# Kernel optimization log

Measured on AMD Instinct MI355X. Metric: run time of the kernel, lower is better.

## Reference

```python
import jax, jax.numpy as jnp
import numpy as np

HEAD_N = 16
EMBED_D = 1024
MASK_FILL = 1e-09  # source uses masked_fill(mask==0, 1e-09), NOT -inf


def setup_inputs() -> dict:
    key = jax.random.key(0)
    ks = jax.random.split(key, 8)
    B, S, D = 4, 4096, EMBED_D
    L = S // HEAD_N
    q = jax.random.normal(ks[0], (B, S, D), dtype=jnp.float32)
    k = jax.random.normal(ks[1], (B, S, D), dtype=jnp.float32)
    v = jax.random.normal(ks[2], (B, S, D), dtype=jnp.float32)
    mask = jax.random.randint(ks[3], (B, L, L), 0, 2, dtype=jnp.int32)
    scale = 0.02
    Wq = jax.random.normal(ks[4], (D, D), dtype=jnp.float32) * scale
    Wk = jax.random.normal(ks[5], (D, D), dtype=jnp.float32) * scale
    Wv = jax.random.normal(ks[6], (D, D), dtype=jnp.float32) * scale
    Wo = jax.random.normal(ks[7], (D, D), dtype=jnp.float32) * scale
    return {"q": q, "k": k, "v": v, "mask": mask, "Wq": Wq, "Wk": Wk, "Wv": Wv, "Wo": Wo}


def _split_heads(x, B):
    # Faithful to source bug: view(B, -1, head_n, embedding_d).transpose(1, 2)
    # -> splits the SEQUENCE dim by head_n; per-head dim stays EMBED_D.
    return x.reshape(B, -1, HEAD_N, EMBED_D).transpose(0, 2, 1, 3)  # [B,h,L,D]


def reference(q, k, v, mask, Wq, Wk, Wv, Wo):
    B, S, D = q.shape
    qh = _split_heads(q @ Wq, B)
    kh = _split_heads(k @ Wk, B)
    vh = _split_heads(v @ Wv, B)
    # score: [B, h, L, L], L = S // head_n
    score = jnp.einsum("bhld,bhmd->bhlm", qh, kh) / jnp.sqrt(jnp.float32(D))
    m = mask[:, None, :, :]  # unsqueeze(1) -> broadcast over heads
    score = jnp.where(m == 0, jnp.float32(MASK_FILL), score)
    att = jax.nn.softmax(score, axis=-1)  # dropout p=0.0 -> identity
    x = jnp.einsum("bhlm,bhmd->bhld", att, vh)  # [B,h,L,D]
    x = x.transpose(0, 2, 1, 3).reshape(B, S, D)
    return x @ Wo
```

## Files before the change

### kernel.cpp

```cpp
#include <hip/hip_runtime.h>
#include <hip/hip_bf16.h>

typedef __bf16 bf16x8 __attribute__((ext_vector_type(8)));
typedef float f32x4 __attribute__((ext_vector_type(4)));
typedef unsigned short ushort_t;
typedef unsigned int uint_t;

#define HN 16
#define LSEQ 256
#define DD 1024
#define BB 4
#define SS 4096
#define MROWS (BB * SS)
#define BHN (BB * HN)

#define AS1 __attribute__((address_space(1)))
#define AS3 __attribute__((address_space(3)))

__device__ __forceinline__ ushort_t f2bf(float f) {
  uint_t u = __builtin_bit_cast(uint_t, f);
  u += 0x7fffu + ((u >> 16) & 1u);
  return (ushort_t)(u >> 16);
}
__device__ __forceinline__ uint_t pk2(float lo, float hi) {
  return (uint_t)f2bf(lo) | ((uint_t)f2bf(hi) << 16);
}

__global__ __launch_bounds__(256) void cvt3(const float4* __restrict__ s0,
                                            const float4* __restrict__ s1,
                                            const float4* __restrict__ s2,
                                            uint4* __restrict__ out) {
  const int z = blockIdx.y;
  const float4* in = (z == 0) ? s0 : (z == 1) ? s1 : s2;
  const long i = (long)blockIdx.x * 256 + threadIdx.x;
  const float4 a = in[i * 2];
  const float4 b = in[i * 2 + 1];
  uint4 o;
  o.x = pk2(a.x, a.y);
  o.y = pk2(a.z, a.w);
  o.z = pk2(b.x, b.y);
  o.w = pk2(b.z, b.w);
  out[(long)z * 2097152 + i] = o;
}

__global__ __launch_bounds__(256) void transpose_w4(const float* __restrict__ W0,
                                                    const float* __restrict__ W1,
                                                    const float* __restrict__ W2,
                                                    const float* __restrict__ W3,
                                                    ushort_t* __restrict__ WT) {
  __shared__ float tile[32][33];
  const int z = blockIdx.z;
  const float* W = (z == 0) ? W0 : (z == 1) ? W1 : (z == 2) ? W2 : W3;
  ushort_t* dst = WT + (long)z * 1048576;
  const int tx = threadIdx.x, ty = threadIdx.y;
  const int bn = blockIdx.x * 32, bk = blockIdx.y * 32;
#pragma unroll
  for (int j = 0; j < 32; j += 8)
    tile[ty + j][tx] = W[(long)(bk + ty + j) * DD + bn + tx];
  __syncthreads();
#pragma unroll
  for (int j = 0; j < 32; j += 8)
    dst[(long)(bn + ty + j) * DD + bk + tx] = f2bf(tile[tx][ty + j]);
}

__global__ __launch_bounds__(256, 2) void score_sm(const ushort_t* __restrict__ qh,
                                                   const ushort_t* __restrict__ kh,
                                                   const int* __restrict__ mask,
                                                   ushort_t* __restrict__ att) {
  __shared__ char smemraw[81920];
  ushort_t* sA = (ushort_t*)smemraw;
  ushort_t* sB = (ushort_t*)(smemraw + 16384);
  float* Sf = (float*)smemraw;

  const int orig = blockIdx.x;
  const int wgid = (orig & 7) * 32 + (orig >> 3);
  const int bh = wgid >> 2, rb = wgid & 3;
  const int b = bh >> 4;
  const ushort_t* A = qh + ((long)bh * 256 + rb * 64) * 1024;
  const ushort_t* Bk = kh + (long)bh * 256 * 1024;

  const int t = threadIdx.x, lane = t & 63, wid = t >> 6;
  const int fr = lane & 15, q = lane >> 4;
  const int wc = wid * 64;
  const int sw0 = (q ^ (fr & 7)) * 8;
  const int sw1 = ((4 + q) ^ (fr & 7)) * 8;

  int srcAo[2], dstA[2], srcBo[8], dstB[8];
#pragma unroll
  for (int i = 0; i < 2; ++i) {
    const int c = i * 256 + t, row = c >> 3, gc = (c & 7) ^ (row & 7);
    srcAo[i] = row * 1024 + gc * 8;
    dstA[i] = (i * 256 + (t & 192)) * 8;
  }
#pragma unroll
  for (int i = 0; i < 8; ++i) {
    const int c = i * 256 + t, row = c >> 3, gc = (c & 7) ^ (row & 7);
    srcBo[i] = row * 1024 + gc * 8;
    dstB[i] = (i * 256 + (t & 192)) * 8;
  }

  auto stage = [&](int buf, int kt) {
    const int ko = kt * 64;
#pragma unroll
    for (int i = 0; i < 2; ++i)
      __builtin_amdgcn_global_load_lds(
          (const AS1 void*)(A + srcAo[i] + ko),
          (AS3 void*)(sA + buf * 4096 + dstA[i]), 16, 0, 0);
#pragma unroll
    for (int i = 0; i < 8; ++i)
      __builtin_amdgcn_global_load_lds(
          (const AS1 void*)(Bk + srcBo[i] + ko),
          (AS3 void*)(sB + buf * 16384 + dstB[i]), 16, 0, 0);
  };

  f32x4 acc[4][4];
#pragma unroll
  for (int m = 0; m < 4; ++m)
#pragma unroll
    for (int n = 0; n < 4; ++n) acc[m][n] = (f32x4){0.f, 0.f, 0.f, 0.f};

  stage(0, 0);
  __syncthreads();
  int cur = 0;
  for (int kt = 0; kt < 16; ++kt) {
    if (kt < 15) stage(cur ^ 1, kt + 1);
    bf16x8 af[4][2], bfv[4][2];
    const ushort_t* bA = sA + cur * 4096;
    const ushort_t* bB = sB + cur * 16384;
#pragma unroll
    for (int m = 0; m < 4; ++m) {
      af[m][0] = *(const bf16x8*)(bA + (m * 16 + fr) * 64 + sw0);
      af[m][1] = *(const bf16x8*)(bA + (m * 16 + fr) * 64 + sw1);
    }
#pragma unroll
    for (int n = 0; n < 4; ++n) {
      bfv[n][0] = *(const bf16x8*)(bB + (wc + n * 16 + fr) * 64 + sw0);
      bfv[n][1] = *(const bf16x8*)(bB + (wc + n * 16 + fr) * 64 + sw1);
    }
#pragma unroll
    for (int m = 0; m < 4; ++m)
#pragma unroll
      for (int n = 0; n < 4; ++n) {
        acc[m][n] = __builtin_amdgcn_mfma_f32_16x16x32_bf16(af[m][0], bfv[n][0], acc[m][n], 0, 0, 0);
        acc[m][n] = __builtin_amdgcn_mfma_f32_16x16x32_bf16(af[m][1], bfv[n][1], acc[m][n], 0, 0, 0);
      }
    __syncthreads();
    cur ^= 1;
  }

#pragma unroll
  for (int m = 0; m < 4; ++m)
#pragma unroll
    for (int n = 0; n < 4; ++n)
#pragma unroll
      for (int r = 0; r < 4; ++r)
        Sf[(m * 16 + q * 4 + r) * 256 + wc + n * 16 + fr] = acc[m][n][r];
  __syncthreads();

#pragma unroll 2
  for (int i = 0; i < 16; ++i) {
    const int row = wid * 16 + i;
    const int gl = rb * 64 + row;
    const f32x4 sv = *(const f32x4*)&Sf[row * 256 + lane * 4];
    const int4 mv = *(const int4*)&mask[((long)b * 256 + gl) * 256 + lane * 4];
    float s[4];
    s[0] = (mv.x == 0) ? 1e-9f : sv[0] * 0.03125f;
    s[1] = (mv.y == 0) ? 1e-9f : sv[1] * 0.03125f;
    s[2] = (mv.z == 0) ? 1e-9f : sv[2] * 0.03125f;
    s[3] = (mv.w == 0) ? 1e-9f : sv[3] * 0.03125f;
    float mx = fmaxf(fmaxf(s[0], s[1]), fmaxf(s[2], s[3]));
#pragma unroll
    for (int off = 32; off; off >>= 1) mx = fmaxf(mx, __shfl_xor(mx, off));
    float e[4], sum = 0.f;
#pragma unroll
    for (int j = 0; j < 4; ++j) {
      e[j] = __expf(s[j] - mx);
      sum += e[j];
    }
#pragma unroll
    for (int off = 32; off; off >>= 1) sum += __shfl_xor(sum, off);
    const float inv = 1.0f / sum;
    ushort4 o;
    o.x = f2bf(e[0] * inv);
    o.y = f2bf(e[1] * inv);
    o.z = f2bf(e[2] * inv);
    o.w = f2bf(e[3] * inv);
    *(ushort4*)&att[((long)bh * 256 + gl) * 256 + lane * 4] = o;
  }
}

__global__ __launch_bounds__(256, 2) void gemm_tn(const ushort_t* __restrict__ Ab,
                                                  const ushort_t* __restrict__ Btp,
                                                  void* __restrict__ Cp, int K, int ldA,
                                                  int ldC, long batchA, long batchB) {
  __shared__ ushort_t smem[16384];
  ushort_t* sA = smem;
  ushort_t* sB = smem + 8192;

  const int bx = blockIdx.x, by = blockIdx.y, z = blockIdx.z;
  const int rowBase = by * 128;
  const int colBase = bx * 128;

  const int t = threadIdx.x;
  const int lane = t & 63;
  const int wid = t >> 6;
  const int wr = (wid >> 1) * 64;
  const int wc = (wid & 1) * 64;
  const int fr = lane & 15;
  const int fk = (lane >> 4) * 8;

  const ushort_t* Atile = Ab + batchA * z + (long)rowBase * ldA;
  const ushort_t* Btile = Btp + batchB * z;

  int sBstat[2];
#pragma unroll
  for (int i = 0; i < 2; ++i) {
    const int c = i * 256 + t;
    const int x8 = (c & 3) * 8;
    sBstat[i] = (x8 >> 4) * 16384 + (colBase + (c >> 2)) * 16 + (x8 & 15);
  }

  f32x4 acc[4][4];
#pragma unroll
  for (int m = 0; m < 4; ++m)
#pragma unroll
    for (int n = 0; n < 4; ++n) acc[m][n] = (f32x4){0.f, 0.f, 0.f, 0.f};

  const int NT = K >> 5;

  auto stageAB = [&](int buf, int kt) {
    const long ko = (long)kt * 32;
#pragma unroll
    for (int i = 0; i < 2; ++i) {
      const int c = i * 256 + t;
      const int cw = i * 256 + (t & 192);
      __builtin_amdgcn_global_load_lds(
          (const AS1 void*)(Atile + (long)(c >> 2) * ldA + ko + (c & 3) * 8),
          (AS3 void*)(sA + buf * 4096 + cw * 8), 16, 0, 0);
      __builtin_amdgcn_global_load_lds(
          (const AS1 void*)(Btile + sBstat[i] + (long)kt * 32768),
          (AS3 void*)(sB + buf * 4096 + cw * 8), 16, 0, 0);
    }
  };

  stageAB(0, 0);
  __syncthreads();

  int cur = 0;
  for (int kt = 0; kt < NT; ++kt) {
    if (kt + 1 < NT) stageAB(cur ^ 1, kt + 1);

    bf16x8 af[4], bfv[4];
    const ushort_t* baseA = sA + cur * 4096 + fk;
    const ushort_t* baseB = sB + cur * 4096 + fk;
#pragma unroll
    for (int m = 0; m < 4; ++m) af[m] = *(const bf16x8*)(baseA + (wr + m * 16 + fr) * 32);
#pragma unroll
    for (int n = 0; n < 4; ++n) bfv[n] = *(const bf16x8*)(baseB + (wc + n * 16 + fr) * 32);

#pragma unroll
    for (int m = 0; m < 4; ++m)
#pragma unroll
      for (int n = 0; n < 4; ++n)
        acc[m][n] = __builtin_amdgcn_mfma_f32_16x16x32_bf16(af[m], bfv[n], acc[m][n], 0, 0, 0);

    __syncthreads();
    cur ^= 1;
  }

  const int rq = (lane >> 4) * 4;
#pragma unroll
  for (int m = 0; m < 4; ++m)
#pragma unroll
    for (int n = 0; n < 4; ++n)
#pragma unroll
      for (int r = 0; r < 4; ++r)
        smem[(wr + m * 16 + rq + r) * 128 + wc + n * 16 + fr] = f2bf(acc[m][n][r]);
  __syncthreads();
  ushort_t* Cb = (ushort_t*)Cp;
  const int c8 = (lane & 15) * 8;
#pragma unroll
  for (int i = 0; i < 8; ++i) {
    const int row = i * 16 + wid * 4 + (lane >> 4);
    const uint4 val = *(const uint4*)(smem + row * 128 + c8);
    const int l = rowBase + row;
    const int orow = ((z >> 4) << 12) + l * 16 + (z & 15);
    *(uint4*)(Cb + (long)orow * 1024 + colBase + c8) = val;
  }
}

#define SBAR() asm volatile("s_barrier" ::: "memory")
#define LGKM0() asm volatile("s_waitcnt lgkmcnt(0)" ::: "memory")
#define VM(N) asm volatile("s_waitcnt vmcnt(" #N ")" ::: "memory")
#define PH_OPEN() SBAR(); LGKM0(); __builtin_amdgcn_s_setprio(1)
#define PH_CLOSE() __builtin_amdgcn_s_setprio(0); SBAR()

template <int SMODE>
__global__ __launch_bounds__(512, 1) void gemm256(const ushort_t* __restrict__ A0,
                                                  const ushort_t* __restrict__ A1,
                                                  const ushort_t* __restrict__ A2,
                                                  const ushort_t* __restrict__ Btp,
                                                  void* __restrict__ Cp, long bStrideZ,
                                                  long cStrideZ, int vzsel) {
  __shared__ ushort_t sm[65536];

  const int orig = blockIdx.x;
  const int cpx = (int)gridDim.x >> 3;
  const int wgid = (orig & 7) * cpx + (orig >> 3);
  const int z = wgid >> 8;
  const int tile = wgid & 255;
  const int by = tile >> 2, bx = tile & 3;
  const int rowBase = by * 256, colBase = bx * 256;

  const ushort_t* Ab = (z == 0) ? A0 : (z == 1) ? A1 : A2;
  const ushort_t* Bt = Btp + bStrideZ * z;

  const int t = threadIdx.x;
  const int lane = t & 63;
  const int wid = t >> 6;
  const int wm = wid >> 2;
  const int wn = wid & 3;
  const int fr = lane & 15;
  const int q = lane >> 4;

  const int sw0 = ((q ^ (fr & 7)) * 8);
  const int sw1 = (((4 + q) ^ (fr & 7)) * 8);
  const int aoff0 = fr * 64 + sw0;
  const int aoff1 = fr * 64 + sw1;
  const int bbase = ((wn & 1) * 64 + fr) * 64;
  const int boff0 = bbase + sw0;
  const int boff1 = bbase + sw1;

  const ushort_t* srcA[2][2];
  const ushort_t* srcB[2][2];
  int ldsoff[2];
#pragma unroll
  for (int i = 0; i < 2; ++i) {
    const int c = i * 512 + t;
    const int rowc = c >> 3;
    const int gc = (c & 7) ^ (rowc & 7);
    srcA[0][i] = Ab + (long)(rowBase + rowc) * 1024 + gc * 8;
    srcA[1][i] = Ab + (long)(rowBase + 128 + rowc) * 1024 + gc * 8;
    srcB[0][i] = Bt + (long)(colBase + rowc) * 1024 + gc * 8;
    srcB[1][i] = Bt + (long)(colBase + 128 + rowc) * 1024 + gc * 8;
    ldsoff[i] = (c & ~63) * 8;
  }

#define STAGE(kind, h, T)                                                                   \
  do {                                                                                      \
    ushort_t* _d = sm + ((kind) ? 32768 : 0) + ((T) & 1) * 16384 + (h) * 8192;              \
    const ushort_t* _s0 = ((kind) ? srcB[h][0] : srcA[h][0]) + (long)(T) * 64;              \
    __builtin_amdgcn_global_load_lds((const AS1 void*)_s0,                                  \
                                     (AS3 void*)(_d + ldsoff[0]), 16, 0, 0);                \
    const ushort_t* _s1 = ((kind) ? srcB[h][1] : srcA[h][1]) + (long)(T) * 64;              \
    __builtin_amdgcn_global_load_lds((const AS1 void*)_s1,                                  \
                                     (AS3 void*)(_d + ldsoff[1]), 16, 0, 0);                \
  } while (0)

  f32x4 acc[8][4];
#pragma unroll
  for (int m = 0; m < 8; ++m)
#pragma unroll
    for (int n = 0; n < 4; ++n) acc[m][n] = (f32x4){0.f, 0.f, 0.f, 0.f};

  bf16x8 af[4][2], bf0[2][2], bf1[2][2];

#define LDA4(dbuf, msub)                                                         \
  do {                                                                           \
    const ushort_t* _b = sm + (dbuf)*16384 + wm * 8192 + (msub)*4096;            \
    _Pragma("unroll") for (int m2 = 0; m2 < 4; ++m2) {                           \
      af[m2][0] = *(const bf16x8*)(_b + m2 * 1024 + aoff0);                      \
      af[m2][1] = *(const bf16x8*)(_b + m2 * 1024 + aoff1);                      \
    }                                                                            \
  } while (0)

#define LDB2(dbuf, nsub, bfv)                                                    \
  do {                                                                           \
    const ushort_t* _b = sm + 32768 + (dbuf)*16384 + (wn >> 1) * 8192 + (nsub)*2048; \
    _Pragma("unroll") for (int n2 = 0; n2 < 2; ++n2) {                           \
      bfv[n2][0] = *(const bf16x8*)(_b + n2 * 1024 + boff0);                     \
      bfv[n2][1] = *(const bf16x8*)(_b + n2 * 1024 + boff1);                     \
    }                                                                            \
  } while (0)

#define MMQ(msub, nsub, bfv)                                                     \
  do {                                                                           \
    _Pragma("unroll") for (int m2 = 0; m2 < 4; ++m2)                             \
        _Pragma("unroll") for (int n2 = 0; n2 < 2; ++n2) {                       \
      acc[(msub)*4 + m2][(nsub)*2 + n2] = __builtin_amdgcn_mfma_f32_16x16x32_bf16( \
          af[m2][0], bfv[n2][0], acc[(msub)*4 + m2][(nsub)*2 + n2], 0, 0, 0);    \
      acc[(msub)*4 + m2][(nsub)*2 + n2] = __builtin_amdgcn_mfma_f32_16x16x32_bf16( \
          af[m2][1], bfv[n2][1], acc[(msub)*4 + m2][(nsub)*2 + n2], 0, 0, 0);    \
    }                                                                            \
  } while (0)

  const int NT = 16;
  const int NI = 8;

  STAGE(0, 0, 0);
  STAGE(0, 1, 0);
  STAGE(1, 0, 0);
  STAGE(1, 1, 0);
  STAGE(0, 0, 1);
  STAGE(0, 1, 1);
  STAGE(1, 0, 1);
  STAGE(1, 1, 1);
  VM(8);
  SBAR();

  for (int it = 0; it < NI - 1; ++it) {
    const int T0 = 2 * it;
    LDA4(0, 0);
    LDB2(0, 0, bf0);
    PH_OPEN(); MMQ(0, 0, bf0); PH_CLOSE();
    LDB2(0, 1, bf1);
    PH_OPEN(); MMQ(0, 1, bf1); PH_CLOSE();
    LDA4(0, 1);
    STAGE(1, 0, T0 + 2);
    STAGE(1, 1, T0 + 2);
    PH_OPEN(); MMQ(1, 1, bf1); PH_CLOSE();
    STAGE(0, 0, T0 + 2);
    STAGE(0, 1, T0 + 2);
    SBAR();
    __builtin_amdgcn_s_setprio(1);
    MMQ(1, 0, bf0);
    __builtin_amdgcn_s_setprio(0);
    VM(8);
    SBAR();
    LDA4(1, 0);
    LDB2(1, 0, bf0);
    PH_OPEN(); MMQ(0, 0, bf0); PH_CLOSE();
    LDB2(1, 1, bf1);
    PH_OPEN(); MMQ(0, 1, bf1); PH_CLOSE();
    LDA4(1, 1);
    STAGE(1, 0, T0 + 3);
    STAGE(1, 1, T0 + 3);
    PH_OPEN(); MMQ(1, 1, bf1); PH_CLOSE();
    STAGE(0, 0, T0 + 3);
    STAGE(0, 1, T0 + 3);
    SBAR();
    __builtin_amdgcn_s_setprio(1);
    MMQ(1, 0, bf0);
    __builtin_amdgcn_s_setprio(0);
    VM(8);
    SBAR();
  }

  {
    LDA4(0, 0);
    LDB2(0, 0, bf0);
    PH_OPEN(); MMQ(0, 0, bf0); PH_CLOSE();
    LDB2(0, 1, bf1);
    PH_OPEN(); MMQ(0, 1, bf1); PH_CLOSE();
    LDA4(0, 1);
    PH_OPEN(); MMQ(1, 1, bf1); PH_CLOSE();
    SBAR();
    __builtin_amdgcn_s_setprio(1);
    MMQ(1, 0, bf0);
    __builtin_amdgcn_s_setprio(0);
    VM(0);
    SBAR();
    LDA4(1, 0);
    LDB2(1, 0, bf0);
    PH_OPEN(); MMQ(0, 0, bf0); PH_CLOSE();
    LDB2(1, 1, bf1);
    PH_OPEN(); MMQ(0, 1, bf1); PH_CLOSE();
    LDA4(1, 1);
    PH_OPEN(); MMQ(1, 1, bf1); PH_CLOSE();
    SBAR();
    MMQ(1, 0, bf0);
    SBAR();
  }

  const int rq = q * 4;
  if constexpr (SMODE == 0) {
    float* Cf = (float*)Cp + cStrideZ * z;
#pragma unroll
    for (int m = 0; m < 8; ++m)
#pragma unroll
      for (int n = 0; n < 4; ++n)
#pragma unroll
        for (int r = 0; r < 4; ++r) {
          const int row = rowBase + wm * 128 + m * 16 + rq + r;
          const int col = colBase + wn * 64 + n * 16 + fr;
          Cf[(long)row * 1024 + col] = acc[m][n][r];
        }
  } else {
#pragma unroll
    for (int m = 0; m < 8; ++m)
#pragma unroll
      for (int n = 0; n < 4; ++n)
#pragma unroll
        for (int r = 0; r < 4; ++r) {
          const int row = wm * 128 + m * 16 + rq + r;
          const int col = wn * 64 + n * 16 + fr;
          sm[row * 256 + (((col >> 3) ^ (row & 7)) * 8) + (col & 7)] = f2bf(acc[m][n][r]);
        }
    __syncthreads();
    ushort_t* Cb = (ushort_t*)Cp + cStrideZ * z;
    if (z != vzsel) {
      const int cc = t & 31;
      const int r0 = t >> 5;
#pragma unroll
      for (int i = 0; i < 16; ++i) {
        const int row = r0 + i * 16;
        const uint4 val = *(const uint4*)(sm + row * 256 + ((cc ^ (row & 7)) * 8));
        const int grow = rowBase + row;
        const int b = grow >> 12;
        const int s = grow & 4095;
        const int orow = ((b << 4) + (s & 15)) * 256 + (s >> 4);
        *(uint4*)(Cb + (long)orow * 1024 + colBase + cc * 8) = val;
      }
    } else {
      const int bq = rowBase >> 12;
      const int lblk = (rowBase & 4095) >> 8;
      ushort_t* base0 = Cb + (long)lblk * 16384;
#pragma unroll
      for (int i = 0; i < 8; ++i) {
        const int cid = i * 512 + t;
        const int d = cid & 255;
        const int h = cid >> 8;
        uint_t w[8];
#pragma unroll
        for (int j = 0; j < 8; ++j) {
          const int r0 = (2 * j) * 16 + h;
          const int r1 = (2 * j + 1) * 16 + h;
          const ushort_t v0 = sm[r0 * 256 + (((d >> 3) ^ (r0 & 7)) * 8) + (d & 7)];
          const ushort_t v1 = sm[r1 * 256 + (((d >> 3) ^ (r1 & 7)) * 8) + (d & 7)];
          w[j] = (uint_t)v0 | ((uint_t)v1 << 16);
        }
        ushort_t* dst = base0 + (long)(bq * 16 + h) * 262144 + (colBase + d) * 16;
        *(uint4*)dst = make_uint4(w[0], w[1], w[2], w[3]);
        *(uint4*)(dst + 8) = make_uint4(w[4], w[5], w[6], w[7]);
      }
    }
  }
#undef STAGE
#undef LDA4
#undef LDB2
#undef MMQ
}

extern "C" void kernel_launch(void* const* d_in, const int* in_sizes, int n_in,
                              void* d_out, int out_size, void* d_ws, size_t ws_size,
                              hipStream_t stream) {
  const float* q = (const float*)d_in[0];
  const float* k = (const float*)d_in[1];
  const float* v = (const float*)d_in[2];
  const int* mask = (const int*)d_in[3];
  const float* Wq = (const float*)d_in[4];
  const float* Wk = (const float*)d_in[5];
  const float* Wv = (const float*)d_in[6];
  const float* Wo = (const float*)d_in[7];
  float* out = (float*)d_out;

  char* ws = (char*)d_ws;
  const size_t MB = 1024 * 1024;
  ushort_t* WT = (ushort_t*)ws;
  const dim3 tb(32, 8);
  transpose_w4<<<dim3(32, 32, 4), tb, 0, stream>>>(Wq, Wk, Wv, Wo, WT);

  const bool big = ws_size >= (size_t)200 * MB;

  if (big) {
    ushort_t* qkvb = (ushort_t*)(ws + 8 * MB);
    ushort_t* qh = (ushort_t*)(ws + 104 * MB);
    ushort_t* kh = (ushort_t*)(ws + 136 * MB);
    ushort_t* vhT2 = (ushort_t*)(ws + 168 * MB);
    ushort_t* att = (ushort_t*)(ws + 40 * MB);
    ushort_t* x = (ushort_t*)(ws + 48 * MB);

    cvt3<<<dim3(8192, 3), 256, 0, stream>>>((const float4*)q, (const float4*)k,
                                            (const float4*)v, (uint4*)qkvb);
    gemm256<1><<<768, 512, 0, stream>>>(qkvb, qkvb + (size_t)16777216,
                                        qkvb + (size_t)33554432, WT, qh, 1 << 20,
                                        (long)16777216, 2);
    score_sm<<<256, 256, 0, stream>>>(qh, kh, mask, att);
    gemm_tn<<<dim3(8, 2, BHN), 256, 0, stream>>>(att, vhT2, x, 256, 256, 1024,
                                                 (long)65536, (long)262144);
    gemm256<0><<<256, 512, 0, stream>>>(x, x, x, WT + (size_t)3145728, out, 0, 0, -1);
  } else {
    ushort_t* qb = (ushort_t*)(ws + 8 * MB);
    ushort_t* qh = (ushort_t*)(ws + 40 * MB);
    ushort_t* kh = (ushort_t*)(ws + 72 * MB);
    ushort_t* vhT2 = (ushort_t*)(ws + 104 * MB);
    ushort_t* att = (ushort_t*)(ws + 8 * MB);
    ushort_t* x = (ushort_t*)(ws + 16 * MB);

    cvt3<<<dim3(8192, 1), 256, 0, stream>>>((const float4*)q, (const float4*)q,
                                            (const float4*)q, (uint4*)qb);
    gemm256<1><<<256, 512, 0, stream>>>(qb, qb, qb, WT, qh, 0, 0, -1);
    cvt3<<<dim3(8192, 1), 256, 0, stream>>>((const float4*)k, (const float4*)k,
                                            (const float4*)k, (uint4*)qb);
    gemm256<1><<<256, 512, 0, stream>>>(qb, qb, qb, WT + (size_t)1048576, kh, 0, 0, -1);
    cvt3<<<dim3(8192, 1), 256, 0, stream>>>((const float4*)v, (const float4*)v,
                                            (const float4*)v, (uint4*)qb);
    gemm256<1><<<256, 512, 0, stream>>>(qb, qb, qb, WT + (size_t)2097152, vhT2, 0, 0, 0);
    score_sm<<<256, 256, 0, stream>>>(qh, kh, mask, att);
    gemm_tn<<<dim3(8, 2, BHN), 256, 0, stream>>>(att, vhT2, x, 256, 256, 1024,
                                                 (long)65536, (long)262144);
    gemm256<0><<<256, 512, 0, stream>>>(x, x, x, WT + (size_t)3145728, out, 0, 0, -1);
  }
}
```

Measured before the change: 257.9 us.

## Fuse score-softmax with PV matmul and merge input prep kernels

The attention-probability matrix now stays in LDS, and each workgroup computes its 64x1024 output slice directly from a double-buffered stream of V tiles. This removes the global round trip of the att buffer and the separate gemm_tn launch. The weight transpose and the q/k/v bf16 conversion are merged into one prep launch. The cost is a larger LDS footprint (112KB) that limits occupancy to one block per CU, with only 256 workgroups. In the small-workspace path, the qb buffer now holds all three converted inputs, which may overlap the qh/kh regions.

```diff
diff --git a/kernel.cpp b/kernel.cpp
--- a/kernel.cpp
+++ b/kernel.cpp
@@ -26,51 +26,60 @@
   return (uint_t)f2bf(lo) | ((uint_t)f2bf(hi) << 16);
 }
 
-__global__ __launch_bounds__(256) void cvt3(const float4* __restrict__ s0,
-                                            const float4* __restrict__ s1,
-                                            const float4* __restrict__ s2,
-                                            uint4* __restrict__ out) {
-  const int z = blockIdx.y;
-  const float4* in = (z == 0) ? s0 : (z == 1) ? s1 : s2;
-  const long i = (long)blockIdx.x * 256 + threadIdx.x;
-  const float4 a = in[i * 2];
-  const float4 b = in[i * 2 + 1];
-  uint4 o;
-  o.x = pk2(a.x, a.y);
-  o.y = pk2(a.z, a.w);
-  o.z = pk2(b.x, b.y);
-  o.w = pk2(b.z, b.w);
-  out[(long)z * 2097152 + i] = o;
+__global__ __launch_bounds__(256) void prep(const float* __restrict__ q,
+                                            const float* __restrict__ k,
+                                            const float* __restrict__ v,
+                                            const float* __restrict__ W0,
+                                            const float* __restrict__ W1,
+                                            const float* __restrict__ W2,
+                                            const float* __restrict__ W3,
+                                            uint4* __restrict__ qkvb,
+                                            ushort_t* __restrict__ WT) {
+  const int bid = blockIdx.x;
+  const int t = threadIdx.x;
+  if (bid < 24576) {
+    const int z = bid >> 13;
+    const float4* in = (const float4*)((z == 0) ? q : (z == 1) ? k : v);
+    const long i = (long)(bid & 8191) * 256 + t;
+    const float4 a = in[i * 2];
+    const float4 b = in[i * 2 + 1];
+    uint4 o;
+    o.x = pk2(a.x, a.y);
+    o.y = pk2(a.z, a.w);
+    o.z = pk2(b.x, b.y);
+    o.w = pk2(b.z, b.w);
+    qkvb[(long)z * 2097152 + i] = o;
+  } else {
+    __shared__ float tile[32][33];
+    const int b2 = bid - 24576;
+    const int z = b2 >> 10;
+    const float* W = (z == 0) ? W0 : (z == 1) ? W1 : (z == 2) ? W2 : W3;
+    ushort_t* dst = WT + (long)z * 1048576;
+    const int rem = b2 & 1023;
+    const int bn = (rem & 31) * 32, bk = (rem >> 5) * 32;
+    const int tx = t & 31, ty = t >> 5;
+#pragma unroll
+    for (int j = 0; j < 32; j += 8)
+      tile[ty + j][tx] = W[(long)(bk + ty + j) * DD + bn + tx];
+    __syncthreads();
+#pragma unroll
+    for (int j = 0; j < 32; j += 8)
+      dst[(long)(bn + ty + j) * DD + bk + tx] = f2bf(tile[tx][ty + j]);
+  }
 }
 
-__global__ __launch_bounds__(256) void transpose_w4(const float* __restrict__ W0,
-                                                    const float* __restrict__ W1,
-                                                    const float* __restrict__ W2,
-                                                    const float* __restrict__ W3,
-                                                    ushort_t* __restrict__ WT) {
-  __shared__ float tile[32][33];
-  const int z = blockIdx.z;
-  const float* W = (z == 0) ? W0 : (z == 1) ? W1 : (z == 2) ? W2 : W3;
-  ushort_t* dst = WT + (long)z * 1048576;
-  const int tx = threadIdx.x, ty = threadIdx.y;
-  const int bn = blockIdx.x * 32, bk = blockIdx.y * 32;
-#pragma unroll
-  for (int j = 0; j < 32; j += 8)
-    tile[ty + j][tx] = W[(long)(bk + ty + j) * DD + bn + tx];
-  __syncthreads();
-#pragma unroll
-  for (int j = 0; j < 32; j += 8)
-    dst[(long)(bn + ty + j) * DD + bk + tx] = f2bf(tile[tx][ty + j]);
-}
-
-__global__ __launch_bounds__(256, 2) void score_sm(const ushort_t* __restrict__ qh,
-                                                   const ushort_t* __restrict__ kh,
-                                                   const int* __restrict__ mask,
-                                                   ushort_t* __restrict__ att) {
-  __shared__ char smemraw[81920];
+__global__ __launch_bounds__(256, 1) void attn_fused(const ushort_t* __restrict__ qh,
+                                                     const ushort_t* __restrict__ kh,
+                                                     const ushort_t* __restrict__ vhT2,
+                                                     const int* __restrict__ mask,
+                                                     ushort_t* __restrict__ x) {
+  __shared__ char smemraw[114688];
   ushort_t* sA = (ushort_t*)smemraw;
   ushort_t* sB = (ushort_t*)(smemraw + 16384);
   float* Sf = (float*)smemraw;
+  ushort_t* sPV = (ushort_t*)smemraw;
+  ushort_t* sC = (ushort_t*)(smemraw + 32768);
+  ushort_t* attL = (ushort_t*)(smemraw + 81920);
 
   const int orig = blockIdx.x;
   const int wgid = (orig & 7) * 32 + (orig >> 3);
@@ -78,6 +87,7 @@
   const int b = bh >> 4;
   const ushort_t* A = qh + ((long)bh * 256 + rb * 64) * 1024;
   const ushort_t* Bk = kh + (long)bh * 256 * 1024;
+  const ushort_t* Vb = vhT2 + (long)bh * 262144;
 
   const int t = threadIdx.x, lane = t & 63, wid = t >> 6;
   const int fr = lane & 15, q = lane >> 4;
@@ -97,6 +107,13 @@
     const int c = i * 256 + t, row = c >> 3, gc = (c & 7) ^ (row & 7);
     srcBo[i] = row * 1024 + gc * 8;
     dstB[i] = (i * 256 + (t & 192)) * 8;
+  }
+  int pvOff[8], pvDst[8];
+#pragma unroll
+  for (int i = 0; i < 8; ++i) {
+    const int c = i * 256 + t, dr = c >> 3, gc = (c & 7) ^ (dr & 7);
+    pvOff[i] = (gc >> 1) * 16384 + dr * 16 + (gc & 1) * 8;
+    pvDst[i] = (i * 256 + (t & 192)) * 8;
   }
 
   auto stage = [&](int buf, int kt) {
@@ -185,107 +202,76 @@
     o.y = f2bf(e[1] * inv);
     o.z = f2bf(e[2] * inv);
     o.w = f2bf(e[3] * inv);
-    *(ushort4*)&att[((long)bh * 256 + gl) * 256 + lane * 4] = o;
-  }
-}
-
-__global__ __launch_bounds__(256, 2) void gemm_tn(const ushort_t* __restrict__ Ab,
-                                                  const ushort_t* __restrict__ Btp,
-                                                  void* __restrict__ Cp, int K, int ldA,
-                                                  int ldC, long batchA, long batchB) {
-  __shared__ ushort_t smem[16384];
-  ushort_t* sA = smem;
-  ushort_t* sB = smem + 8192;
-
-  const int bx = blockIdx.x, by = blockIdx.y, z = blockIdx.z;
-  const int rowBase = by * 128;
-  const int colBase = bx * 128;
-
-  const int t = threadIdx.x;
-  const int lane = t & 63;
-  const int wid = t >> 6;
-  const int wr = (wid >> 1) * 64;
-  const int wc = (wid & 1) * 64;
-  const int fr = lane & 15;
-  const int fk = (lane >> 4) * 8;
-
-  const ushort_t* Atile = Ab + batchA * z + (long)rowBase * ldA;
-  const ushort_t* Btile = Btp + batchB * z;
-
-  int sBstat[2];
-#pragma unroll
-  for (int i = 0; i < 2; ++i) {
-    const int c = i * 256 + t;
-    const int x8 = (c & 3) * 8;
-    sBstat[i] = (x8 >> 4) * 16384 + (colBase + (c >> 2)) * 16 + (x8 & 15);
-  }
-
-  f32x4 acc[4][4];
-#pragma unroll
-  for (int m = 0; m < 4; ++m)
-#pragma unroll
-    for (int n = 0; n < 4; ++n) acc[m][n] = (f32x4){0.f, 0.f, 0.f, 0.f};
-
-  const int NT = K >> 5;
-
-  auto stageAB = [&](int buf, int kt) {
-    const long ko = (long)kt * 32;
-#pragma unroll
-    for (int i = 0; i < 2; ++i) {
-      const int c = i * 256 + t;
-      const int cw = i * 256 + (t & 192);
+    const int mch = lane >> 1;
+    *(ushort4*)(attL + row * 256 + (((mch ^ (row & 7)) << 3) + (lane & 1) * 4)) = o;
+  }
+  __syncthreads();
+
+  const int r0 = t >> 2, qd = t & 3;
+  const long orow = (long)((b << 12) + (rb * 64 + r0) * 16 + (bh & 15));
+  for (int nb = 0; nb < 4; ++nb) {
+#pragma unroll
+    for (int m = 0; m < 4; ++m)
+#pragma unroll
+      for (int n = 0; n < 4; ++n) acc[m][n] = (f32x4){0.f, 0.f, 0.f, 0.f};
+
+#pragma unroll
+    for (int i = 0; i < 8; ++i)
       __builtin_amdgcn_global_load_lds(
-          (const AS1 void*)(Atile + (long)(c >> 2) * ldA + ko + (c & 3) * 8),
-          (AS3 void*)(sA + buf * 4096 + cw * 8), 16, 0, 0);
-      __builtin_amdgcn_global_load_lds(
-          (const AS1 void*)(Btile + sBstat[i] + (long)kt * 32768),
-          (AS3 void*)(sB + buf * 4096 + cw * 8), 16, 0, 0);
+          (const AS1 void*)(Vb + pvOff[i] + nb * 4096),
+          (AS3 void*)(sPV + pvDst[i]), 16, 0, 0);
+    __syncthreads();
+
+    int pbuf = 0;
+    for (int mt = 0; mt < 4; ++mt) {
+      if (mt < 3) {
+#pragma unroll
+        for (int i = 0; i < 8; ++i)
+          __builtin_amdgcn_global_load_lds(
+              (const AS1 void*)(Vb + pvOff[i] + (mt + 1) * 65536 + nb * 4096),
+              (AS3 void*)(sPV + (pbuf ^ 1) * 16384 + pvDst[i]), 16, 0, 0);
+      }
+#pragma unroll
+      for (int kk = 0; kk < 2; ++kk) {
+        bf16x8 af[4], bfv[4];
+#pragma unroll
+        for (int m = 0; m < 4; ++m) {
+          const int l = m * 16 + fr;
+          af[m] = *(const bf16x8*)(attL + l * 256 + (((mt * 8 + kk * 4 + q) ^ (l & 7)) << 3));
+        }
+#pragma unroll
+        for (int n = 0; n < 4; ++n) {
+          const int dr = wc + n * 16 + fr;
+          bfv[n] = *(const bf16x8*)(sPV + pbuf * 16384 + dr * 64 + (((kk * 4 + q) ^ (dr & 7)) << 3));
+        }
+#pragma unroll
+        for (int m = 0; m < 4; ++m)
+#pragma unroll
+          for (int n = 0; n < 4; ++n)
+            acc[m][n] = __builtin_amdgcn_mfma_f32_16x16x32_bf16(af[m], bfv[n], acc[m][n], 0, 0, 0);
+      }
+      __syncthreads();
+      pbuf ^= 1;
     }
-  };
-
-  stageAB(0, 0);
-  __syncthreads();
-
-  int cur = 0;
-  for (int kt = 0; kt < NT; ++kt) {
-    if (kt + 1 < NT) stageAB(cur ^ 1, kt + 1);
-
-    bf16x8 af[4], bfv[4];
-    const ushort_t* baseA = sA + cur * 4096 + fk;
-    const ushort_t* baseB = sB + cur * 4096 + fk;
-#pragma unroll
-    for (int m = 0; m < 4; ++m) af[m] = *(const bf16x8*)(baseA + (wr + m * 16 + fr) * 32);
-#pragma unroll
-    for (int n = 0; n < 4; ++n) bfv[n] = *(const bf16x8*)(baseB + (wc + n * 16 + fr) * 32);
 
 #pragma unroll
     for (int m = 0; m < 4; ++m)
 #pragma unroll
       for (int n = 0; n < 4; ++n)
-        acc[m][n] = __builtin_amdgcn_mfma_f32_16x16x32_bf16(af[m], bfv[n], acc[m][n], 0, 0, 0);
-
+#pragma unroll
+        for (int r = 0; r < 4; ++r) {
+          const int row = m * 16 + q * 4 + r;
+          const int col = wc + n * 16 + fr;
+          sC[row * 256 + (((col >> 3) ^ (row & 7)) << 3) + (col & 7)] = f2bf(acc[m][n][r]);
+        }
     __syncthreads();
-    cur ^= 1;
-  }
-
-  const int rq = (lane >> 4) * 4;
-#pragma unroll
-  for (int m = 0; m < 4; ++m)
-#pragma unroll
-    for (int n = 0; n < 4; ++n)
-#pragma unroll
-      for (int r = 0; r < 4; ++r)
-        smem[(wr + m * 16 + rq + r) * 128 + wc + n * 16 + fr] = f2bf(acc[m][n][r]);
-  __syncthreads();
-  ushort_t* Cb = (ushort_t*)Cp;
-  const int c8 = (lane & 15) * 8;
-#pragma unroll
-  for (int i = 0; i < 8; ++i) {
-    const int row = i * 16 + wid * 4 + (lane >> 4);
-    const uint4 val = *(const uint4*)(smem + row * 128 + c8);
-    const int l = rowBase + row;
-    const int orow = ((z >> 4) << 12) + l * 16 + (z & 15);
-    *(uint4*)(Cb + (long)orow * 1024 + colBase + c8) = val;
+    ushort_t* dst = x + orow * 1024 + nb * 256 + qd * 64;
+#pragma unroll
+    for (int j = 0; j < 8; ++j) {
+      const int cc = qd * 8 + j;
+      *(uint4*)(dst + j * 8) = *(const uint4*)(sC + r0 * 256 + ((cc ^ (r0 & 7)) << 3));
+    }
+    __syncthreads();
   }
 }
 
@@ -557,8 +543,6 @@
   char* ws = (char*)d_ws;
   const size_t MB = 1024 * 1024;
   ushort_t* WT = (ushort_t*)ws;
-  const dim3 tb(32, 8);
-  transpose_w4<<<dim3(32, 32, 4), tb, 0, stream>>>(Wq, Wk, Wv, Wo, WT);
 
   const bool big = ws_size >= (size_t)200 * MB;
 
@@ -567,38 +551,28 @@
     ushort_t* qh = (ushort_t*)(ws + 104 * MB);
     ushort_t* kh = (ushort_t*)(ws + 136 * MB);
     ushort_t* vhT2 = (ushort_t*)(ws + 168 * MB);
-    ushort_t* att = (ushort_t*)(ws + 40 * MB);
     ushort_t* x = (ushort_t*)(ws + 48 * MB);
 
-    cvt3<<<dim3(8192, 3), 256, 0, stream>>>((const float4*)q, (const float4*)k,
-                                            (const float4*)v, (uint4*)qkvb);
+    prep<<<28672, 256, 0, stream>>>(q, k, v, Wq, Wk, Wv, Wo, (uint4*)qkvb, WT);
     gemm256<1><<<768, 512, 0, stream>>>(qkvb, qkvb + (size_t)16777216,
                                         qkvb + (size_t)33554432, WT, qh, 1 << 20,
                                         (long)16777216, 2);
-    score_sm<<<256, 256, 0, stream>>>(qh, kh, mask, att);
-    gemm_tn<<<dim3(8, 2, BHN), 256, 0, stream>>>(att, vhT2, x, 256, 256, 1024,
-                                                 (long)65536, (long)262144);
+    attn_fused<<<256, 256, 0, stream>>>(qh, kh, vhT2, mask, x);
     gemm256<0><<<256, 512, 0, stream>>>(x, x, x, WT + (size_t)3145728, out, 0, 0, -1);
   } else {
     ushort_t* qb = (ushort_t*)(ws + 8 * MB);
     ushort_t* qh = (ushort_t*)(ws + 40 * MB);
     ushort_t* kh = (ushort_t*)(ws + 72 * MB);
     ushort_t* vhT2 = (ushort_t*)(ws + 104 * MB);
-    ushort_t* att = (ushort_t*)(ws + 8 * MB);
     ushort_t* x = (ushort_t*)(ws + 16 * MB);
 
-    cvt3<<<dim3(8192, 1), 256, 0, stream>>>((const float4*)q, (const float4*)q,
-                                            (const float4*)q, (uint4*)qb);
+    prep<<<28672, 256, 0, stream>>>(q, k, v, Wq, Wk, Wv, Wo, (uint4*)qb, WT);
     gemm256<1><<<256, 512, 0, stream>>>(qb, qb, qb, WT, qh, 0, 0, -1);
-    cvt3<<<dim3(8192, 1), 256, 0, stream>>>((const float4*)k, (const float4*)k,
-                                            (const float4*)k, (uint4*)qb);
-    gemm256<1><<<256, 512, 0, stream>>>(qb, qb, qb, WT + (size_t)1048576, kh, 0, 0, -1);
-    cvt3<<<dim3(8192, 1), 256, 0, stream>>>((const float4*)v, (const float4*)v,
-                                            (const float4*)v, (uint4*)qb);
-    gemm256<1><<<256, 512, 0, stream>>>(qb, qb, qb, WT + (size_t)2097152, vhT2, 0, 0, 0);
-    score_sm<<<256, 256, 0, stream>>>(qh, kh, mask, att);
-    gemm_tn<<<dim3(8, 2, BHN), 256, 0, stream>>>(att, vhT2, x, 256, 256, 1024,
-                                                 (long)65536, (long)262144);
+    gemm256<1><<<256, 512, 0, stream>>>(qb + (size_t)16777216, qb + (size_t)16777216,
+                                        qb + (size_t)16777216, WT + (size_t)1048576, kh, 0, 0, -1);
+    gemm256<1><<<256, 512, 0, stream>>>(qb + (size_t)33554432, qb + (size_t)33554432,
+                                        qb + (size_t)33554432, WT + (size_t)2097152, vhT2, 0, 0, 0);
+    attn_fused<<<256, 256, 0, stream>>>(qh, kh, vhT2, mask, x);
     gemm256<0><<<256, 512, 0, stream>>>(x, x, x, WT + (size_t)3145728, out, 0, 0, -1);
   }
 }
```

Measured after the change: 256.7 us. About the same (-0.5%).
